# Performance work log

Measured on AMD Instinct MI355X. Metric: run time of the kernel, lower is better.

The kernel has to match this reference:

```python
import jax, jax.numpy as jnp
import numpy as np

N_HEAD = 16
T_THRESHOLD = 0.001


def setup_inputs() -> dict:
    key = jax.random.key(0)
    k_x, k_wa, k_ba, k_wp, k_bp = jax.random.split(key, 5)
    B, P, L, R = 8, 1024, 4, 256
    C = L * R  # n_embd = 1024
    s = 1.0 / np.sqrt(C)
    return {
        "x": jax.random.normal(k_x, (B, P, L, R), dtype=jnp.float32),
        "w_attn": jax.random.normal(k_wa, (C, 3 * C), dtype=jnp.float32) * s,
        "b_attn": jax.random.normal(k_ba, (3 * C,), dtype=jnp.float32) * 0.01,
        "w_proj": jax.random.normal(k_wp, (C, C), dtype=jnp.float32) * s,
        "b_proj": jax.random.normal(k_bp, (C,), dtype=jnp.float32) * 0.01,
    }


def reference(x, w_attn, b_attn, w_proj, b_proj):
    B, P, L, R = x.shape
    C = L * R
    H = N_HEAD
    hd = C // H
    xf = x.reshape(B, P, C)                      # (B, T, C)
    qkv = xf @ w_attn + b_attn                   # (B, T, 3C)
    q, k, v = jnp.split(qkv, 3, axis=-1)
    # (B, H, T, hd)
    q = q.reshape(B, P, H, hd).transpose(0, 2, 1, 3)
    k = k.reshape(B, P, H, hd).transpose(0, 2, 1, 3)
    v = v.reshape(B, P, H, hd).transpose(0, 2, 1, 3)
    att = jnp.einsum("bhqd,bhkd->bhqk", q, k) * (1.0 / np.sqrt(hd))
    att = jax.nn.softmax(att, axis=-1)
    att = jax.nn.relu(att - T_THRESHOLD)         # post-softmax thresholding
    y = jnp.einsum("bhqk,bhkd->bhqd", att, v)    # (B, H, T, hd)
    y = y.transpose(0, 2, 1, 3).reshape(B, P, C)
    y = y @ w_proj + b_proj
    return y.reshape(B, P, L, R)
```

## Files before the change

### kernel.cpp

```cpp
#include <hip/hip_runtime.h>


typedef _Float16 half8 __attribute__((ext_vector_type(8)));
typedef _Float16 half4_t __attribute__((ext_vector_type(4)));
typedef float floatx4 __attribute__((ext_vector_type(4)));

__device__ __forceinline__ void gl2lds16(const void* gsrc, void* lds) {
    __builtin_amdgcn_global_load_lds(
        (const __attribute__((address_space(1))) unsigned int*)gsrc,
        (__attribute__((address_space(3))) unsigned int*)lds,
        16, 0, 0);
}

__global__ __launch_bounds__(256) void conv_x(const float4* __restrict__ in,
                                              _Float16* __restrict__ out, int n4) {
    int idx = blockIdx.x * blockDim.x + threadIdx.x;
    int stride = gridDim.x * blockDim.x;
    for (int i = idx; i < n4; i += stride) {
        float4 v = in[i];
        half4_t h = { (_Float16)v.x, (_Float16)v.y, (_Float16)v.z, (_Float16)v.w };
        *(half4_t*)(out + (size_t)i * 4) = h;
    }
}

__global__ __launch_bounds__(256) void tconv(const float* __restrict__ in,
                                             _Float16* __restrict__ out, int R, int C) {
    __shared__ _Float16 t[64 * 65];
    int bx = blockIdx.x, by = blockIdx.y;
#pragma unroll
    for (int it = 0; it < 16; ++it) {
        int idx = it * 256 + threadIdx.x;
        int r = idx >> 6, c = idx & 63;
        t[c * 65 + r] = (_Float16)in[(size_t)(by * 64 + r) * C + bx * 64 + c];
    }
    __syncthreads();
#pragma unroll
    for (int it = 0; it < 16; ++it) {
        int idx = it * 256 + threadIdx.x;
        int rn = idx >> 6, ck = idx & 63;
        out[(size_t)(bx * 64 + rn) * R + by * 64 + ck] = t[rn * 65 + ck];
    }
}

template <bool SPLIT3>
__global__ __launch_bounds__(256) void gemm_tn(const _Float16* __restrict__ A,
                                               const _Float16* __restrict__ BT,
                                               const float* __restrict__ bias,
                                               void* __restrict__ o0, void* __restrict__ o1,
                                               void* __restrict__ o2, int N) {
    constexpr int K = 1024;
    __shared__ __attribute__((aligned(16))) _Float16 sA[128 * 32];
    __shared__ __attribute__((aligned(16))) _Float16 sB[128 * 32];
    int tid = threadIdx.x;
    int W = tid >> 6, lane = tid & 63, quad = lane >> 4, l15 = lane & 15;
    int m0 = blockIdx.y * 128, n0 = blockIdx.x * 128;
    int wr = (W >> 1) * 64, wc = (W & 1) * 64;
    floatx4 acc[4][4] = {};

    for (int kt = 0; kt < K / 32; ++kt) {
        int k0 = kt * 32;
#pragma unroll
        for (int rho = 0; rho < 2; ++rho) {
            int lin = rho * 256 + tid;
            const _Float16* gA = A + (size_t)(m0 + (lin >> 2)) * K + k0 + (lin & 3) * 8;
            const _Float16* gB = BT + (size_t)(n0 + (lin >> 2)) * K + k0 + (lin & 3) * 8;
            int ldsoff = __builtin_amdgcn_readfirstlane((rho * 256 + W * 64) * 16);
            gl2lds16(gA, (char*)sA + ldsoff);
            gl2lds16(gB, (char*)sB + ldsoff);
        }
        __syncthreads();
        half8 a[4], b[4];
#pragma unroll
        for (int rf = 0; rf < 4; ++rf)
            a[rf] = *(const half8*)(sA + (wr + rf * 16 + l15) * 32 + quad * 8);
#pragma unroll
        for (int cf = 0; cf < 4; ++cf)
            b[cf] = *(const half8*)(sB + (wc + cf * 16 + l15) * 32 + quad * 8);
#pragma unroll
        for (int rf = 0; rf < 4; ++rf)
#pragma unroll
            for (int cf = 0; cf < 4; ++cf)
                acc[rf][cf] = __builtin_amdgcn_mfma_f32_16x16x32_f16(a[rf], b[cf], acc[rf][cf], 0, 0, 0);
        __syncthreads();
    }
    int sec = SPLIT3 ? (n0 >> 10) : 0;
#pragma unroll
    for (int cf = 0; cf < 4; ++cf) {
        int gn = n0 + wc + cf * 16 + l15;
        float bv = bias[gn];
        int cn = gn & 1023;
        int hh = cn >> 6, dd = cn & 63;
#pragma unroll
        for (int rf = 0; rf < 4; ++rf) {
            int gmBase = m0 + wr + rf * 16 + quad * 4;
#pragma unroll
            for (int r = 0; r < 4; ++r) {
                float v = acc[rf][cf][r] + bv;
                int gm = gmBase + r;
                if (!SPLIT3) {
                    ((float*)o0)[(size_t)gm * N + gn] = v;
                } else if (sec == 0) {
                    ((_Float16*)o0)[(size_t)gm * 1024 + cn] = (_Float16)v;
                } else {
                    int b = gm >> 10, t = gm & 1023;
                    int bh = b * 16 + hh;
                    if (sec == 1) {
                        size_t idx = (size_t)bh * 65536 + (t >> 4) * 1024 + (dd >> 5) * 512 +
                                     ((dd >> 3) & 3) * 128 + (t & 15) * 8 + (dd & 7);
                        ((_Float16*)o1)[idx] = (_Float16)v;
                    } else {
                        size_t idx = (size_t)bh * 65536 + (t >> 5) * 2048 + (dd >> 4) * 512 +
                                     ((t >> 3) & 3) * 128 + (dd & 15) * 8 + (t & 7);
                        ((_Float16*)o2)[idx] = (_Float16)v;
                    }
                }
            }
        }
    }
}

__device__ __forceinline__ int esw(int row, int colByte) {
    return row * 2048 + (colByte ^ ((row & 7) << 4));
}

__global__ __launch_bounds__(512, 4) void attn(const _Float16* __restrict__ qn,
                                               const _Float16* __restrict__ kP,
                                               const _Float16* __restrict__ vP,
                                               _Float16* __restrict__ y) {
    __shared__ __attribute__((aligned(16))) _Float16 E[32 * 1024];
    __shared__ float lsum[8][32];
    char* Eb = (char*)E;
    int tid = threadIdx.x;
    int W = tid >> 6, lane = tid & 63, quad = lane >> 4, l15 = lane & 15;
    int qt = blockIdx.x, bh = blockIdx.y;
    int b = bh >> 4, h = bh & 15;
    int q0 = qt * 32;

    half8 bq[2][2];
#pragma unroll
    for (int nf = 0; nf < 2; ++nf)
#pragma unroll
        for (int ks = 0; ks < 2; ++ks)
            bq[nf][ks] = *(const half8*)(qn + (size_t)(b * 1024 + q0 + nf * 16 + l15) * 1024 +
                                         h * 64 + ks * 32 + quad * 8);

    float lpart[2] = {0.f, 0.f};
#pragma unroll 4
    for (int mt = 0; mt < 8; ++mt) {
        int kb = W * 8 + mt;
        const _Float16* kp = kP + ((size_t)(bh * 64 + kb) * 128 + lane) * 8;
        half8 ak0 = *(const half8*)(kp);
        half8 ak1 = *(const half8*)(kp + 512);
#pragma unroll
        for (int nf = 0; nf < 2; ++nf) {
            floatx4 s = {};
            s = __builtin_amdgcn_mfma_f32_16x16x32_f16(ak0, bq[nf][0], s, 0, 0, 0);
            s = __builtin_amdgcn_mfma_f32_16x16x32_f16(ak1, bq[nf][1], s, 0, 0, 0);
            half4_t h4;
#pragma unroll
            for (int r = 0; r < 4; ++r) {
                float e = __expf(fminf(s[r] * 0.125f, 10.0f));
                lpart[nf] += e;
                h4[r] = (_Float16)e;
            }
            int q = nf * 16 + l15;
            int kbyte = (W * 128 + mt * 16 + quad * 4) * 2;
            *(half4_t*)(Eb + q * 2048 + (kbyte ^ ((q & 7) << 4))) = h4;
        }
    }
#pragma unroll
    for (int nf = 0; nf < 2; ++nf) {
        lpart[nf] += __shfl_xor(lpart[nf], 16);
        lpart[nf] += __shfl_xor(lpart[nf], 32);
    }
    if (lane < 16) {
        lsum[W][l15] = lpart[0];
        lsum[W][16 + l15] = lpart[1];
    }
    __syncthreads();

    {
        int rf = W & 1, cf = W >> 1;
        float l = 0.f;
#pragma unroll
        for (int w = 0; w < 8; ++w) l += lsum[w][rf * 16 + l15];
        _Float16 invh = (_Float16)(1.0f / l);
        half8 inv8, t8, z8;
#pragma unroll
        for (int j = 0; j < 8; ++j) { inv8[j] = invh; t8[j] = (_Float16)(-0.001f); z8[j] = (_Float16)0.f; }

        const _Float16* vb = vP + ((size_t)bh * 65536 + cf * 512 + quad * 128 + l15 * 8);
        int erow = rf * 16 + l15;
        floatx4 acc0 = {}, acc1 = {};
#pragma unroll 4
        for (int kt = 0; kt < 32; kt += 2) {
            half8 ap0 = *(const half8*)(Eb + esw(erow, (kt * 32 + quad * 8) * 2));
            half8 bv0 = *(const half8*)(vb + kt * 2048);
            half8 ap1 = *(const half8*)(Eb + esw(erow, ((kt + 1) * 32 + quad * 8) * 2));
            half8 bv1 = *(const half8*)(vb + (kt + 1) * 2048);
            ap0 = __builtin_elementwise_max(ap0 * inv8 + t8, z8);
            ap1 = __builtin_elementwise_max(ap1 * inv8 + t8, z8);
            acc0 = __builtin_amdgcn_mfma_f32_16x16x32_f16(ap0, bv0, acc0, 0, 0, 0);
            acc1 = __builtin_amdgcn_mfma_f32_16x16x32_f16(ap1, bv1, acc1, 0, 0, 0);
        }
        acc0 += acc1;
#pragma unroll
        for (int r = 0; r < 4; ++r) {
            int q = q0 + rf * 16 + quad * 4 + r;
            int d = h * 64 + cf * 16 + l15;
            y[(size_t)(b * 1024 + q) * 1024 + d] = (_Float16)acc0[r];
        }
    }
}

extern "C" void kernel_launch(void* const* d_in, const int* in_sizes, int n_in,
                              void* d_out, int out_size, void* d_ws, size_t ws_size,
                              hipStream_t stream) {
    const float* x  = (const float*)d_in[0];
    const float* wa = (const float*)d_in[1];
    const float* ba = (const float*)d_in[2];
    const float* wp = (const float*)d_in[3];
    const float* bp = (const float*)d_in[4];
    float* out = (float*)d_out;

    char* ws = (char*)d_ws;
    _Float16* xh  = (_Float16*)(ws);
    _Float16* qn  = (_Float16*)(ws + 16777216);
    _Float16* vP  = (_Float16*)(ws + 33554432);
    _Float16* y   = (_Float16*)(ws + 50331648);
    _Float16* kP  = (_Float16*)(ws + 67108864);
    _Float16* waT = (_Float16*)(ws + 83886080);
    _Float16* wpT = (_Float16*)(ws + 90177536);

    conv_x<<<4096, 256, 0, stream>>>((const float4*)x, xh, 8388608 / 4);
    tconv<<<dim3(48, 16), 256, 0, stream>>>(wa, waT, 1024, 3072);
    tconv<<<dim3(16, 16), 256, 0, stream>>>(wp, wpT, 1024, 1024);
    gemm_tn<true><<<dim3(24, 64), 256, 0, stream>>>(xh, waT, ba, (void*)qn, (void*)kP, (void*)vP, 3072);
    attn<<<dim3(32, 128), 512, 0, stream>>>(qn, kP, vP, y);
    gemm_tn<false><<<dim3(8, 64), 256, 0, stream>>>(y, wpT, bp, (void*)out, nullptr, nullptr, 1024);
}
```

Baseline: 293.3 us.

## Merge prep kernels into one launch and vectorize GEMM epilogue stores

Three preprocessing launches (x fp32->fp16 convert and two weight transposes) are folded into a single prep kernel that dispatches on block index, removing two launches and their gaps. The GEMM now swaps the MFMA operand order for the q, k and output sections so each lane holds four consecutive columns. That lets the epilogue use vector bias loads and 4-wide half or float stores instead of scalar scattered stores. The v section keeps the original orientation but packs four consecutive t values into one half4 store, matching its permuted layout. Risks are more code paths and possible index mismatches in the packed layouts.

```diff
diff --git a/kernel.cpp b/kernel.cpp
--- a/kernel.cpp
+++ b/kernel.cpp
@@ -12,33 +12,49 @@
         16, 0, 0);
 }
 
-__global__ __launch_bounds__(256) void conv_x(const float4* __restrict__ in,
-                                              _Float16* __restrict__ out, int n4) {
-    int idx = blockIdx.x * blockDim.x + threadIdx.x;
-    int stride = gridDim.x * blockDim.x;
-    for (int i = idx; i < n4; i += stride) {
-        float4 v = in[i];
-        half4_t h = { (_Float16)v.x, (_Float16)v.y, (_Float16)v.z, (_Float16)v.w };
-        *(half4_t*)(out + (size_t)i * 4) = h;
-    }
-}
-
-__global__ __launch_bounds__(256) void tconv(const float* __restrict__ in,
-                                             _Float16* __restrict__ out, int R, int C) {
-    __shared__ _Float16 t[64 * 65];
-    int bx = blockIdx.x, by = blockIdx.y;
+__device__ __forceinline__ void tconv_body(const float* __restrict__ in,
+                                           _Float16* __restrict__ out,
+                                           int bx, int by, int R, int C,
+                                           _Float16 (*t)[ 65 * 64]) {
+    _Float16* tt = (_Float16*)t;
 #pragma unroll
     for (int it = 0; it < 16; ++it) {
         int idx = it * 256 + threadIdx.x;
         int r = idx >> 6, c = idx & 63;
-        t[c * 65 + r] = (_Float16)in[(size_t)(by * 64 + r) * C + bx * 64 + c];
+        tt[c * 65 + r] = (_Float16)in[(size_t)(by * 64 + r) * C + bx * 64 + c];
     }
     __syncthreads();
 #pragma unroll
     for (int it = 0; it < 16; ++it) {
         int idx = it * 256 + threadIdx.x;
         int rn = idx >> 6, ck = idx & 63;
-        out[(size_t)(bx * 64 + rn) * R + by * 64 + ck] = t[rn * 65 + ck];
+        out[(size_t)(bx * 64 + rn) * R + by * 64 + ck] = tt[rn * 65 + ck];
+    }
+}
+
+__global__ __launch_bounds__(256) void prep(const float* __restrict__ x,
+                                            const float* __restrict__ wa,
+                                            const float* __restrict__ wp,
+                                            _Float16* __restrict__ xh,
+                                            _Float16* __restrict__ waT,
+                                            _Float16* __restrict__ wpT) {
+    __shared__ _Float16 t[64 * 65];
+    int bid = blockIdx.x;
+    if (bid < 4096) {
+        const float4* in = (const float4*)x;
+        int idx = bid * 256 + threadIdx.x;
+#pragma unroll
+        for (int i = idx; i < 2097152; i += 1048576) {
+            float4 v = in[i];
+            half4_t h = { (_Float16)v.x, (_Float16)v.y, (_Float16)v.z, (_Float16)v.w };
+            *(half4_t*)(xh + (size_t)i * 4) = h;
+        }
+    } else if (bid < 4864) {
+        int tb = bid - 4096;
+        tconv_body(wa, waT, tb % 48, tb / 48, 1024, 3072, (_Float16(*)[65 * 64])t);
+    } else {
+        int tb = bid - 4864;
+        tconv_body(wp, wpT, tb % 16, tb / 16, 1024, 1024, (_Float16(*)[65 * 64])t);
     }
 }
 
@@ -55,6 +71,8 @@
     int W = tid >> 6, lane = tid & 63, quad = lane >> 4, l15 = lane & 15;
     int m0 = blockIdx.y * 128, n0 = blockIdx.x * 128;
     int wr = (W >> 1) * 64, wc = (W & 1) * 64;
+    int sec = SPLIT3 ? (n0 >> 10) : 0;
+    bool vsec = SPLIT3 && sec == 2;
     floatx4 acc[4][4] = {};
 
     for (int kt = 0; kt < K / 32; ++kt) {
@@ -76,44 +94,67 @@
 #pragma unroll
         for (int cf = 0; cf < 4; ++cf)
             b[cf] = *(const half8*)(sB + (wc + cf * 16 + l15) * 32 + quad * 8);
-#pragma unroll
-        for (int rf = 0; rf < 4; ++rf)
-#pragma unroll
-            for (int cf = 0; cf < 4; ++cf)
-                acc[rf][cf] = __builtin_amdgcn_mfma_f32_16x16x32_f16(a[rf], b[cf], acc[rf][cf], 0, 0, 0);
+        if (vsec) {
+#pragma unroll
+            for (int rf = 0; rf < 4; ++rf)
+#pragma unroll
+                for (int cf = 0; cf < 4; ++cf)
+                    acc[rf][cf] = __builtin_amdgcn_mfma_f32_16x16x32_f16(a[rf], b[cf], acc[rf][cf], 0, 0, 0);
+        } else {
+#pragma unroll
+            for (int rf = 0; rf < 4; ++rf)
+#pragma unroll
+                for (int cf = 0; cf < 4; ++cf)
+                    acc[rf][cf] = __builtin_amdgcn_mfma_f32_16x16x32_f16(b[cf], a[rf], acc[rf][cf], 0, 0, 0);
+        }
         __syncthreads();
     }
-    int sec = SPLIT3 ? (n0 >> 10) : 0;
-#pragma unroll
-    for (int cf = 0; cf < 4; ++cf) {
-        int gn = n0 + wc + cf * 16 + l15;
-        float bv = bias[gn];
-        int cn = gn & 1023;
-        int hh = cn >> 6, dd = cn & 63;
-#pragma unroll
-        for (int rf = 0; rf < 4; ++rf) {
-            int gmBase = m0 + wr + rf * 16 + quad * 4;
-#pragma unroll
-            for (int r = 0; r < 4; ++r) {
-                float v = acc[rf][cf][r] + bv;
-                int gm = gmBase + r;
+
+    if (!vsec) {
+#pragma unroll
+        for (int cf = 0; cf < 4; ++cf) {
+            int gnBase = n0 + wc + cf * 16 + quad * 4;
+            floatx4 b4 = *(const floatx4*)(bias + gnBase);
+#pragma unroll
+            for (int rf = 0; rf < 4; ++rf) {
+                int gm = m0 + wr + rf * 16 + l15;
+                floatx4 v = acc[rf][cf] + b4;
                 if (!SPLIT3) {
-                    ((float*)o0)[(size_t)gm * N + gn] = v;
-                } else if (sec == 0) {
-                    ((_Float16*)o0)[(size_t)gm * 1024 + cn] = (_Float16)v;
+                    *(floatx4*)((float*)o0 + (size_t)gm * N + gnBase) = v;
                 } else {
-                    int b = gm >> 10, t = gm & 1023;
-                    int bh = b * 16 + hh;
-                    if (sec == 1) {
-                        size_t idx = (size_t)bh * 65536 + (t >> 4) * 1024 + (dd >> 5) * 512 +
-                                     ((dd >> 3) & 3) * 128 + (t & 15) * 8 + (dd & 7);
-                        ((_Float16*)o1)[idx] = (_Float16)v;
+                    half4_t hv = { (_Float16)v[0], (_Float16)v[1], (_Float16)v[2], (_Float16)v[3] };
+                    int cn0 = gnBase & 1023;
+                    if (sec == 0) {
+                        *(half4_t*)((_Float16*)o0 + (size_t)gm * 1024 + cn0) = hv;
                     } else {
-                        size_t idx = (size_t)bh * 65536 + (t >> 5) * 2048 + (dd >> 4) * 512 +
-                                     ((t >> 3) & 3) * 128 + (dd & 15) * 8 + (t & 7);
-                        ((_Float16*)o2)[idx] = (_Float16)v;
+                        int hh = cn0 >> 6, dd0 = cn0 & 63;
+                        int b = gm >> 10, t = gm & 1023;
+                        size_t idx = (size_t)(b * 16 + hh) * 65536 + (t >> 4) * 1024 +
+                                     (dd0 >> 5) * 512 + ((dd0 >> 3) & 3) * 128 +
+                                     (t & 15) * 8 + (dd0 & 7);
+                        *(half4_t*)((_Float16*)o1 + idx) = hv;
                     }
                 }
+            }
+        }
+    } else {
+#pragma unroll
+        for (int cf = 0; cf < 4; ++cf) {
+            int gn = n0 + wc + cf * 16 + l15;
+            float bv = bias[gn];
+            int cn = gn & 1023;
+            int hh = cn >> 6, dd = cn & 63;
+#pragma unroll
+            for (int rf = 0; rf < 4; ++rf) {
+                int gmBase = m0 + wr + rf * 16 + quad * 4;
+                int b = gmBase >> 10, t0 = gmBase & 1023;
+                half4_t hv;
+#pragma unroll
+                for (int r = 0; r < 4; ++r) hv[r] = (_Float16)(acc[rf][cf][r] + bv);
+                size_t idx = (size_t)(b * 16 + hh) * 65536 + (t0 >> 5) * 2048 +
+                             (dd >> 4) * 512 + ((t0 >> 3) & 3) * 128 +
+                             (dd & 15) * 8 + (t0 & 7);
+                *(half4_t*)((_Float16*)o2 + idx) = hv;
             }
         }
     }
@@ -232,9 +273,7 @@
     _Float16* waT = (_Float16*)(ws + 83886080);
     _Float16* wpT = (_Float16*)(ws + 90177536);
 
-    conv_x<<<4096, 256, 0, stream>>>((const float4*)x, xh, 8388608 / 4);
-    tconv<<<dim3(48, 16), 256, 0, stream>>>(wa, waT, 1024, 3072);
-    tconv<<<dim3(16, 16), 256, 0, stream>>>(wp, wpT, 1024, 1024);
+    prep<<<5120, 256, 0, stream>>>(x, wa, wp, xh, waT, wpT);
     gemm_tn<true><<<dim3(24, 64), 256, 0, stream>>>(xh, waT, ba, (void*)qn, (void*)kP, (void*)vP, 3072);
     attn<<<dim3(32, 128), 512, 0, stream>>>(qn, kP, vP, y);
     gemm_tn<false><<<dim3(8, 64), 256, 0, stream>>>(y, wpT, bp, (void*)out, nullptr, nullptr, 1024);
```

After: 297.9 us. Within noise of the previous version (+1.6%).
